# Performance work log

Measured on AMD Instinct MI355X. Metric: run time of the kernel, lower is better.

Reference implementation:

```python
import jax, jax.numpy as jnp
import numpy as np

H = 16  # hidden_size
I = 30  # GRU input_size (hard-coded in module)


def setup_inputs() -> dict:
    key = jax.random.key(0)
    ks = jax.random.split(key, 12)
    B, T = 4096, 512
    s = lambda k, sh: jax.random.normal(k, sh, jnp.float32) * 0.1
    return {
        "x": jax.random.normal(ks[0], (B, T, I), jnp.float32),
        "lengths": jax.random.randint(ks[1], (B,), 1, T + 1),  # valid lengths in [1, T]
        "w_ih": s(ks[2], (3 * H, I)),
        "w_hh": s(ks[3], (3 * H, H)),
        "b_ih": s(ks[4], (3 * H,)),
        "b_hh": s(ks[5], (3 * H,)),
        "fc1_w": s(ks[6], (H, H)), "fc1_b": s(ks[7], (H,)),
        "fc2_w": s(ks[8], (H, H)), "fc2_b": s(ks[9], (H,)),
        "fc3_w": s(ks[10], (H, H)), "fc3_b": s(ks[11], (H,)),
    }


def _gru_last_hidden(x, lengths, w_ih, w_hh, b_ih, b_hh):
    """Run GRU over padded [B,T,I] and return hidden at t = lengths-1 per row.
    Equivalent to pack_padded -> GRU -> pad_packed -> gather output[b, len-1],
    since h_t only depends on steps <= t."""
    B, T, _ = x.shape
    # Precompute input-side gate activations for all steps: [B,T,3H]
    xg = jnp.einsum('bti,gi->btg', x, w_ih) + b_ih
    xr, xz, xn = jnp.split(xg, 3, axis=-1)
    w_hr, w_hz, w_hn = jnp.split(w_hh, 3, axis=0)
    b_hr, b_hz, b_hn = jnp.split(b_hh, 3)
    tidx = lengths - 1  # [B]

    def step(carry, inp):
        h, last = carry
        t, xr_t, xz_t, xn_t = inp
        r = jax.nn.sigmoid(xr_t + h @ w_hr.T + b_hr)
        z = jax.nn.sigmoid(xz_t + h @ w_hz.T + b_hz)
        n = jnp.tanh(xn_t + r * (h @ w_hn.T + b_hn))
        h = (1.0 - z) * n + z * h
        last = jnp.where((tidx == t)[:, None], h, last)  # capture h at final valid step
        return (h, last), None

    h0 = jnp.zeros((B, H), x.dtype)
    (_, last), _ = jax.lax.scan(
        step, (h0, h0),
        (jnp.arange(T),
         xr.transpose(1, 0, 2), xz.transpose(1, 0, 2), xn.transpose(1, 0, 2)))
    return last  # [B,H]


def reference(x, lengths, w_ih, w_hh, b_ih, b_hh,
              fc1_w, fc1_b, fc2_w, fc2_b, fc3_w, fc3_b):
    h = _gru_last_hidden(x, lengths, w_ih, w_hh, b_ih, b_hh)
    e = h @ fc1_w.T + fc1_b
    e = jax.nn.relu(e) @ fc2_w.T + fc2_b   # dropout is identity in eval mode
    e = jax.nn.relu(e) @ fc3_w.T + fc3_b
    return e
```

## Files before the change

### kernel.cpp

```cpp
#include <hip/hip_runtime.h>
#include <cstdint>
#include <cstddef>

typedef float v2f __attribute__((ext_vector_type(2)));

#define HID 16
#define IN  30

#define FAST_RCP(x) __builtin_amdgcn_rcpf(x)

__device__ __forceinline__ float bperm(int baddr, float v) {
    return __int_as_float(__builtin_amdgcn_ds_bpermute(baddr, __float_as_int(v)));
}
__device__ __forceinline__ float dq1(float v) {
    return __int_as_float(__builtin_amdgcn_mov_dpp(__float_as_int(v), 0xB1, 0xF, 0xF, true));
}
__device__ __forceinline__ float dq2(float v) {
    return __int_as_float(__builtin_amdgcn_mov_dpp(__float_as_int(v), 0x4E, 0xF, 0xF, true));
}
#define PKFMA(acc, a, b) asm("v_pk_fma_f32 %0, %1, %2, %0" : "+v"(acc) : "v"(a), "v"(b))
#define PKMUL(d, a, b)   asm("v_pk_mul_f32 %0, %1, %2"     : "=v"(d)   : "v"(a), "v"(b))

typedef __attribute__((address_space(3))) unsigned int       lds_u32_t;
typedef const __attribute__((address_space(1))) unsigned int glb_u32_t;
#define GLOAD_LDS(gp, lp) \
    __builtin_amdgcn_global_load_lds((glb_u32_t*)(gp), (lds_u32_t*)(lp), 4, 0, 0)

__global__ void k_hist(const int* __restrict__ len, int* __restrict__ hist, int B, int T) {
    int i = blockIdx.x * 256 + threadIdx.x;
    if (i < B) atomicAdd(hist + (T - len[i]), 1);
}
__global__ __launch_bounds__(512) void k_scan(const int* __restrict__ hist, int* __restrict__ off) {
    __shared__ int s[512];
    int t = threadIdx.x;
    int v = hist[t];
    s[t] = v; __syncthreads();
    int acc = v;
    for (int o = 1; o < 512; o <<= 1) {
        int add = (t >= o) ? s[t - o] : 0;
        __syncthreads();
        acc += add; s[t] = acc;
        __syncthreads();
    }
    off[t] = acc - v;
}
__global__ void k_scatter(const int* __restrict__ len, int* __restrict__ off,
                          int* __restrict__ perm, int B, int T) {
    int i = blockIdx.x * 256 + threadIdx.x;
    if (i < B) {
        int b = T - len[i];
        int p = atomicAdd(off + b, 1);
        perm[p] = i;
    }
}

__global__ __launch_bounds__(256, 4) void gru_enc_kernel(
    const float* __restrict__ x, const int* __restrict__ lengths,
    const float* __restrict__ w_ih, const float* __restrict__ w_hh,
    const float* __restrict__ b_ih, const float* __restrict__ b_hh,
    const float* __restrict__ fc1w, const float* __restrict__ fc1b,
    const float* __restrict__ fc2w, const float* __restrict__ fc2b,
    const float* __restrict__ fc3w, const float* __restrict__ fc3b,
    float* __restrict__ out, const int* __restrict__ perm,
    int B, int T)
{
    __shared__ __align__(16) float lds[4][1024];

    const int lane = threadIdx.x & 63;
    const int wib  = threadIdx.x >> 6;
    const int q    = lane & 3;
    const int j    = lane >> 2;

    const int pos = blockIdx.x * 4 + wib;
    if (pos >= B) return;

    const int row = perm ? perm[pos] : pos;
    const int len = lengths[row];

    const float L2E = 1.4426950408889634f;
    const float gsc[3] = { -L2E, -L2E, 2.0f * L2E };

    v2f wih2[3][4];
#pragma unroll
    for (int g = 0; g < 3; ++g) {
        const float* wr = w_ih + (size_t)(g * HID + j) * IN;
#pragma unroll
        for (int m = 0; m < 4; ++m) {
            int p0 = q * 8 + 2 * m;
            v2f t;
            t.x = (p0     < IN) ? wr[p0]     * gsc[g] : 0.0f;
            t.y = (p0 + 1 < IN) ? wr[p0 + 1] * gsc[g] : 0.0f;
            wih2[g][m] = t;
        }
    }
    v2f whh2[3][2];
#pragma unroll
    for (int g = 0; g < 3; ++g)
#pragma unroll
        for (int m = 0; m < 2; ++m) {
            const float* wr = w_hh + (size_t)(g * HID + j) * HID + q * 4 + 2 * m;
            v2f t; t.x = wr[0] * gsc[g]; t.y = wr[1] * gsc[g];
            whh2[g][m] = t;
        }

    const float bR  = -L2E * (b_ih[j] + b_hh[j]);
    const float bZ  = -L2E * (b_ih[HID + j] + b_hh[HID + j]);
    const float biN = 2.0f * L2E * b_ih[2 * HID + j];
    const float bhN = 2.0f * L2E * b_hh[2 * HID + j];

    const int word  = min(lane & 31, 29);
    const int sstep = lane >> 5;
    const float* xrow = x + (size_t)row * T * IN;
    const int tcap = T - 1;

    float* ldsw = &lds[wib][0];
    const float* ldsr = ldsw + q * 8;

    int ba[4];
#pragma unroll
    for (int m = 0; m < 4; ++m) ba[m] = (16 * q + 4 * m) << 2;

#define STAGE(cc) do {                                                     \
        const int t0_ = (cc) << 3;                                         \
        float* lb_ = ldsw + (((cc) & 3) << 8);                             \
        _Pragma("unroll")                                                  \
        for (int i_ = 0; i_ < 4; ++i_) {                                   \
            int ts_ = min(t0_ + (i_ << 1) + sstep, tcap);                  \
            GLOAD_LDS(xrow + (size_t)ts_ * IN + word, lb_ + (i_ << 6));    \
        }                                                                  \
    } while (0)

#define STEP(cw, s) do {                                                    \
        v2f xv0 = *(const v2f*)((cw) + ((s) << 5));                         \
        v2f xv1 = *(const v2f*)((cw) + ((s) << 5) + 2);                     \
        v2f xv2 = *(const v2f*)((cw) + ((s) << 5) + 4);                     \
        v2f xv3 = *(const v2f*)((cw) + ((s) << 5) + 6);                     \
        v2f ar, az, an, hn;                                                 \
        PKMUL(ar, wih2[0][0], xv0);                                         \
        PKMUL(az, wih2[1][0], xv0);                                         \
        PKMUL(an, wih2[2][0], xv0);                                         \
        PKFMA(ar, wih2[0][1], xv1); PKFMA(az, wih2[1][1], xv1);             \
        PKFMA(an, wih2[2][1], xv1);                                         \
        PKFMA(ar, wih2[0][2], xv2); PKFMA(az, wih2[1][2], xv2);             \
        PKFMA(an, wih2[2][2], xv2);                                         \
        PKFMA(ar, wih2[0][3], xv3); PKFMA(az, wih2[1][3], xv3);             \
        PKFMA(an, wih2[2][3], xv3);                                         \
        PKMUL(hn, whh2[2][0], hb2[0]); PKFMA(hn, whh2[2][1], hb2[1]);       \
        PKFMA(ar, whh2[0][0], hb2[0]); PKFMA(ar, whh2[0][1], hb2[1]);       \
        PKFMA(az, whh2[1][0], hb2[0]); PKFMA(az, whh2[1][1], hb2[1]);       \
        float pr  = ar.x + ar.y;  pr  += dq1(pr);  pr  += dq2(pr);          \
        float pz  = az.x + az.y;  pz  += dq1(pz);  pz  += dq2(pz);          \
        float pxn = an.x + an.y;  pxn += dq1(pxn); pxn += dq2(pxn);         \
        float phn = hn.x + hn.y;  phn += dq1(phn); phn += dq2(phn);         \
        float rg = FAST_RCP(1.0f + __builtin_exp2f(pr + bR));               \
        float zg = FAST_RCP(1.0f + __builtin_exp2f(pz + bZ));               \
        float yy = fmaf(rg, phn + bhN, pxn + biN);                          \
        float ng = fmaf(-2.0f, FAST_RCP(1.0f + __builtin_exp2f(yy)), 1.0f); \
        h_own = fmaf(zg, h_own - ng, ng);                                   \
        hb2[0].x = bperm(ba[0], h_own); hb2[0].y = bperm(ba[1], h_own);     \
        hb2[1].x = bperm(ba[2], h_own); hb2[1].y = bperm(ba[3], h_own);     \
    } while (0)

    v2f hb2[2];
    hb2[0].x = 0.0f; hb2[0].y = 0.0f; hb2[1].x = 0.0f; hb2[1].y = 0.0f;
    float h_own = 0.0f;

    const int nfull = len >> 3;
    const int rem   = len & 7;

    STAGE(0); STAGE(1); STAGE(2);

    int c = 0;
    for (; c < nfull; ++c) {
        asm volatile("s_waitcnt vmcnt(8)" ::: "memory");
        STAGE(c + 3);
        const float* cw = ldsr + ((c & 3) << 8);
        STEP(cw, 0); STEP(cw, 1); STEP(cw, 2); STEP(cw, 3);
        STEP(cw, 4); STEP(cw, 5); STEP(cw, 6); STEP(cw, 7);
    }
    if (rem) {
        asm volatile("s_waitcnt vmcnt(8)" ::: "memory");
        const float* cw = ldsr + ((c & 3) << 8);
#pragma unroll
        for (int s = 0; s < 8; ++s) {
            if (s >= rem) break;
            STEP(cw, s);
        }
    }

    float hv[16];
#pragma unroll
    for (int k = 0; k < 16; ++k) hv[k] = __shfl(h_own, 4 * k, 64);

    float e1 = fc1b[j];
#pragma unroll
    for (int k = 0; k < 16; ++k) e1 = fmaf(fc1w[j * HID + k], hv[k], e1);

    float v1[16];
#pragma unroll
    for (int k = 0; k < 16; ++k) v1[k] = fmaxf(__shfl(e1, 4 * k, 64), 0.0f);

    float e2 = fc2b[j];
#pragma unroll
    for (int k = 0; k < 16; ++k) e2 = fmaf(fc2w[j * HID + k], v1[k], e2);

    float v2a[16];
#pragma unroll
    for (int k = 0; k < 16; ++k) v2a[k] = fmaxf(__shfl(e2, 4 * k, 64), 0.0f);

    float e3 = fc3b[j];
#pragma unroll
    for (int k = 0; k < 16; ++k) e3 = fmaf(fc3w[j * HID + k], v2a[k], e3);

    if (q == 0) out[(size_t)row * HID + j] = e3;
}

extern "C" void kernel_launch(void* const* d_in, const int* in_sizes, int n_in,
                              void* d_out, int out_size, void* d_ws, size_t ws_size,
                              hipStream_t stream) {
    const float* x    = (const float*)d_in[0];
    const int*   lens = (const int*)d_in[1];
    const float* w_ih = (const float*)d_in[2];
    const float* w_hh = (const float*)d_in[3];
    const float* b_ih = (const float*)d_in[4];
    const float* b_hh = (const float*)d_in[5];
    const float* fc1w = (const float*)d_in[6];
    const float* fc1b = (const float*)d_in[7];
    const float* fc2w = (const float*)d_in[8];
    const float* fc2b = (const float*)d_in[9];
    const float* fc3w = (const float*)d_in[10];
    const float* fc3b = (const float*)d_in[11];
    float* out = (float*)d_out;

    const int B = in_sizes[1];
    const int T = (int)(in_sizes[0] / ((size_t)B * IN));

    int* wsI = (int*)d_ws;
    const size_t need = ((size_t)B + 1024) * sizeof(int);
    const bool dosort = (ws_size >= need) && (T <= 512) && (T >= 8);
    int* perm = dosort ? wsI : nullptr;
    int* hist = wsI + B;
    int* off  = wsI + B + 512;

    if (dosort) {
        hipMemsetAsync(hist, 0, 512 * sizeof(int), stream);
        k_hist<<<(B + 255) / 256, 256, 0, stream>>>(lens, hist, B, T);
        k_scan<<<1, 512, 0, stream>>>(hist, off);
        k_scatter<<<(B + 255) / 256, 256, 0, stream>>>(lens, off, perm, B, T);
    }

    const int nblk = (B + 3) / 4;
    gru_enc_kernel<<<nblk, 256, 0, stream>>>(x, lens, w_ih, w_hh, b_ih, b_hh,
                                             fc1w, fc1b, fc2w, fc2b, fc3w, fc3b,
                                             out, perm, B, T);
}
```

Before: 173.1 us.

## Replace LDS-staged x pipeline with direct register prefetch, one wave per block

Drops the global_load_lds staging through shared memory and the vmcnt-gated 8-step chunk pipeline. Each lane now loads its own x slice straight into registers, prefetched four timesteps ahead in a rotating set of four buffers, and the q=3 lane's weights and offsets are remapped so no padding lanes are needed. Blocks shrink to a single 64-thread wave, one per batch row, removing the LDS footprint. The cost is more global load instructions per step issued from every lane, and latency hiding now rests on a four-step register prefetch depth.

After: 205.4 us. 1.19x slower.

```diff
diff --git a/kernel.cpp b/kernel.cpp
--- a/kernel.cpp
+++ b/kernel.cpp
@@ -20,11 +20,6 @@
 }
 #define PKFMA(acc, a, b) asm("v_pk_fma_f32 %0, %1, %2, %0" : "+v"(acc) : "v"(a), "v"(b))
 #define PKMUL(d, a, b)   asm("v_pk_mul_f32 %0, %1, %2"     : "=v"(d)   : "v"(a), "v"(b))
-
-typedef __attribute__((address_space(3))) unsigned int       lds_u32_t;
-typedef const __attribute__((address_space(1))) unsigned int glb_u32_t;
-#define GLOAD_LDS(gp, lp) \
-    __builtin_amdgcn_global_load_lds((glb_u32_t*)(gp), (lds_u32_t*)(lp), 4, 0, 0)
 
 __global__ void k_hist(const int* __restrict__ len, int* __restrict__ hist, int B, int T) {
     int i = blockIdx.x * 256 + threadIdx.x;
@@ -54,7 +49,7 @@
     }
 }
 
-__global__ __launch_bounds__(256, 4) void gru_enc_kernel(
+__global__ __launch_bounds__(64, 4) void gru_enc_kernel(
     const float* __restrict__ x, const int* __restrict__ lengths,
     const float* __restrict__ w_ih, const float* __restrict__ w_hh,
     const float* __restrict__ b_ih, const float* __restrict__ b_hh,
@@ -64,18 +59,16 @@
     float* __restrict__ out, const int* __restrict__ perm,
     int B, int T)
 {
-    __shared__ __align__(16) float lds[4][1024];
-
     const int lane = threadIdx.x & 63;
-    const int wib  = threadIdx.x >> 6;
     const int q    = lane & 3;
     const int j    = lane >> 2;
 
-    const int pos = blockIdx.x * 4 + wib;
+    const int pos = blockIdx.x;
     if (pos >= B) return;
 
     const int row = perm ? perm[pos] : pos;
     const int len = lengths[row];
+    const int lenm1 = len - 1;
 
     const float L2E = 1.4426950408889634f;
     const float gsc[3] = { -L2E, -L2E, 2.0f * L2E };
@@ -86,10 +79,15 @@
         const float* wr = w_ih + (size_t)(g * HID + j) * IN;
 #pragma unroll
         for (int m = 0; m < 4; ++m) {
-            int p0 = q * 8 + 2 * m;
+            int p0; bool zer = false;
+            if (q < 3) p0 = q * 8 + 2 * m;
+            else if (m == 0) p0 = 24;
+            else if (m == 1) p0 = 26;
+            else if (m == 2) { p0 = 0; zer = true; }
+            else p0 = 28;
             v2f t;
-            t.x = (p0     < IN) ? wr[p0]     * gsc[g] : 0.0f;
-            t.y = (p0 + 1 < IN) ? wr[p0 + 1] * gsc[g] : 0.0f;
+            t.x = zer ? 0.0f : wr[p0]     * gsc[g];
+            t.y = zer ? 0.0f : wr[p0 + 1] * gsc[g];
             wih2[g][m] = t;
         }
     }
@@ -108,43 +106,37 @@
     const float biN = 2.0f * L2E * b_ih[2 * HID + j];
     const float bhN = 2.0f * L2E * b_hh[2 * HID + j];
 
-    const int word  = min(lane & 31, 29);
-    const int sstep = lane >> 5;
-    const float* xrow = x + (size_t)row * T * IN;
-    const int tcap = T - 1;
-
-    float* ldsw = &lds[wib][0];
-    const float* ldsr = ldsw + q * 8;
-
-    int ba[4];
-#pragma unroll
-    for (int m = 0; m < 4; ++m) ba[m] = (16 * q + 4 * m) << 2;
-
-#define STAGE(cc) do {                                                     \
-        const int t0_ = (cc) << 3;                                         \
-        float* lb_ = ldsw + (((cc) & 3) << 8);                             \
-        _Pragma("unroll")                                                  \
-        for (int i_ = 0; i_ < 4; ++i_) {                                   \
-            int ts_ = min(t0_ + (i_ << 1) + sstep, tcap);                  \
-            GLOAD_LDS(xrow + (size_t)ts_ * IN + word, lb_ + (i_ << 6));    \
-        }                                                                  \
+    const int voff0 = (q < 3) ? q * 32      : 96;
+    const int voff1 = (q < 3) ? q * 32 + 8  : 104;
+    const int voff2 = (q < 3) ? q * 32 + 16 : 112;
+    const int voff3 = (q < 3) ? q * 32 + 24 : 112;
+
+    const char* xrow = (const char*)(x + (size_t)row * T * IN);
+
+    const int ba0 = (16 * q +  0) << 2;
+    const int ba1 = (16 * q +  4) << 2;
+    const int ba2 = (16 * q +  8) << 2;
+    const int ba3 = (16 * q + 12) << 2;
+
+#define LOADT(XB, tt) do {                                                  \
+        const char* p_ = xrow + (size_t)min((tt), lenm1) * (IN * 4);        \
+        XB[0] = *(const v2f*)(p_ + voff0);                                  \
+        XB[1] = *(const v2f*)(p_ + voff1);                                  \
+        XB[2] = *(const v2f*)(p_ + voff2);                                  \
+        XB[3] = *(const v2f*)(p_ + voff3);                                  \
     } while (0)
 
-#define STEP(cw, s) do {                                                    \
-        v2f xv0 = *(const v2f*)((cw) + ((s) << 5));                         \
-        v2f xv1 = *(const v2f*)((cw) + ((s) << 5) + 2);                     \
-        v2f xv2 = *(const v2f*)((cw) + ((s) << 5) + 4);                     \
-        v2f xv3 = *(const v2f*)((cw) + ((s) << 5) + 6);                     \
+#define STEP(XB) do {                                                       \
         v2f ar, az, an, hn;                                                 \
-        PKMUL(ar, wih2[0][0], xv0);                                         \
-        PKMUL(az, wih2[1][0], xv0);                                         \
-        PKMUL(an, wih2[2][0], xv0);                                         \
-        PKFMA(ar, wih2[0][1], xv1); PKFMA(az, wih2[1][1], xv1);             \
-        PKFMA(an, wih2[2][1], xv1);                                         \
-        PKFMA(ar, wih2[0][2], xv2); PKFMA(az, wih2[1][2], xv2);             \
-        PKFMA(an, wih2[2][2], xv2);                                         \
-        PKFMA(ar, wih2[0][3], xv3); PKFMA(az, wih2[1][3], xv3);             \
-        PKFMA(an, wih2[2][3], xv3);                                         \
+        PKMUL(ar, wih2[0][0], XB[0]);                                       \
+        PKMUL(az, wih2[1][0], XB[0]);                                       \
+        PKMUL(an, wih2[2][0], XB[0]);                                       \
+        PKFMA(ar, wih2[0][1], XB[1]); PKFMA(az, wih2[1][1], XB[1]);         \
+        PKFMA(an, wih2[2][1], XB[1]);                                       \
+        PKFMA(ar, wih2[0][2], XB[2]); PKFMA(az, wih2[1][2], XB[2]);         \
+        PKFMA(an, wih2[2][2], XB[2]);                                       \
+        PKFMA(ar, wih2[0][3], XB[3]); PKFMA(az, wih2[1][3], XB[3]);         \
+        PKFMA(an, wih2[2][3], XB[3]);                                       \
         PKMUL(hn, whh2[2][0], hb2[0]); PKFMA(hn, whh2[2][1], hb2[1]);       \
         PKFMA(ar, whh2[0][0], hb2[0]); PKFMA(ar, whh2[0][1], hb2[1]);       \
         PKFMA(az, whh2[1][0], hb2[0]); PKFMA(az, whh2[1][1], hb2[1]);       \
@@ -157,36 +149,27 @@
         float yy = fmaf(rg, phn + bhN, pxn + biN);                          \
         float ng = fmaf(-2.0f, FAST_RCP(1.0f + __builtin_exp2f(yy)), 1.0f); \
         h_own = fmaf(zg, h_own - ng, ng);                                   \
-        hb2[0].x = bperm(ba[0], h_own); hb2[0].y = bperm(ba[1], h_own);     \
-        hb2[1].x = bperm(ba[2], h_own); hb2[1].y = bperm(ba[3], h_own);     \
+        hb2[0].x = bperm(ba0, h_own); hb2[0].y = bperm(ba1, h_own);         \
+        hb2[1].x = bperm(ba2, h_own); hb2[1].y = bperm(ba3, h_own);         \
     } while (0)
 
     v2f hb2[2];
     hb2[0].x = 0.0f; hb2[0].y = 0.0f; hb2[1].x = 0.0f; hb2[1].y = 0.0f;
     float h_own = 0.0f;
 
-    const int nfull = len >> 3;
-    const int rem   = len & 7;
-
-    STAGE(0); STAGE(1); STAGE(2);
-
-    int c = 0;
-    for (; c < nfull; ++c) {
-        asm volatile("s_waitcnt vmcnt(8)" ::: "memory");
-        STAGE(c + 3);
-        const float* cw = ldsr + ((c & 3) << 8);
-        STEP(cw, 0); STEP(cw, 1); STEP(cw, 2); STEP(cw, 3);
-        STEP(cw, 4); STEP(cw, 5); STEP(cw, 6); STEP(cw, 7);
-    }
-    if (rem) {
-        asm volatile("s_waitcnt vmcnt(8)" ::: "memory");
-        const float* cw = ldsr + ((c & 3) << 8);
-#pragma unroll
-        for (int s = 0; s < 8; ++s) {
-            if (s >= rem) break;
-            STEP(cw, s);
-        }
-    }
+    v2f X0[4], X1[4], X2[4], X3[4];
+    LOADT(X0, 0); LOADT(X1, 1); LOADT(X2, 2); LOADT(X3, 3);
+
+    int t = 0;
+    for (; t + 4 <= len; t += 4) {
+        STEP(X0); LOADT(X0, t + 4);
+        STEP(X1); LOADT(X1, t + 5);
+        STEP(X2); LOADT(X2, t + 6);
+        STEP(X3); LOADT(X3, t + 7);
+    }
+    if (t     < len) STEP(X0);
+    if (t + 1 < len) STEP(X1);
+    if (t + 2 < len) STEP(X2);
 
     float hv[16];
 #pragma unroll
@@ -237,7 +220,7 @@
 
     int* wsI = (int*)d_ws;
     const size_t need = ((size_t)B + 1024) * sizeof(int);
-    const bool dosort = (ws_size >= need) && (T <= 512) && (T >= 8);
+    const bool dosort = (ws_size >= need) && (T <= 512) && (T >= 1);
     int* perm = dosort ? wsI : nullptr;
     int* hist = wsI + B;
     int* off  = wsI + B + 512;
@@ -249,8 +232,7 @@
         k_scatter<<<(B + 255) / 256, 256, 0, stream>>>(lens, off, perm, B, T);
     }
 
-    const int nblk = (B + 3) / 4;
-    gru_enc_kernel<<<nblk, 256, 0, stream>>>(x, lens, w_ih, w_hh, b_ih, b_hh,
-                                             fc1w, fc1b, fc2w, fc2b, fc3w, fc3b,
-                                             out, perm, B, T);
-}
+    gru_enc_kernel<<<B, 64, 0, stream>>>(x, lens, w_ih, w_hh, b_ih, b_hh,
+                                         fc1w, fc1b, fc2w, fc2b, fc3w, fc3b,
+                                         out, perm, B, T);
+}
```

## Broadcast hidden state via readlane and pair long/short rows per block

Applied to the files above, without the earlier changes.

Replaces the ds_bpermute exchange of the hidden state and the packed partial dot products with 16 v_readlane broadcasts into scalar registers. Each lane then computes a full 16-wide recurrent dot product per gate from weights held in registers, which removes the LDS-permute latency from the serial dependency chain. The trade-off is more VALU work and more registers per lane. Separately, each block now takes two rows from the front of the length-sorted order and two from the back, pairing long and short sequences so the work per block is more even. The duplicate guard on the back half looks questionable, and the sort is now also enabled for short T.

Result: slower. 298.3 us (+72.3%).

```diff
diff --git a/kernel.cpp b/kernel.cpp
--- a/kernel.cpp
+++ b/kernel.cpp
@@ -9,9 +9,6 @@
 
 #define FAST_RCP(x) __builtin_amdgcn_rcpf(x)
 
-__device__ __forceinline__ float bperm(int baddr, float v) {
-    return __int_as_float(__builtin_amdgcn_ds_bpermute(baddr, __float_as_int(v)));
-}
 __device__ __forceinline__ float dq1(float v) {
     return __int_as_float(__builtin_amdgcn_mov_dpp(__float_as_int(v), 0xB1, 0xF, 0xF, true));
 }
@@ -62,7 +59,7 @@
     const float* __restrict__ fc2w, const float* __restrict__ fc2b,
     const float* __restrict__ fc3w, const float* __restrict__ fc3b,
     float* __restrict__ out, const int* __restrict__ perm,
-    int B, int T)
+    int B, int T, int nblk)
 {
     __shared__ __align__(16) float lds[4][1024];
 
@@ -71,8 +68,11 @@
     const int q    = lane & 3;
     const int j    = lane >> 2;
 
-    const int pos = blockIdx.x * 4 + wib;
-    if (pos >= B) return;
+    int pos;
+    if (wib < 2) pos = 2 * blockIdx.x + wib;
+    else         pos = B - 2 - 2 * blockIdx.x + (wib - 2);
+    if (pos < 0 || pos >= B) return;
+    if (wib >= 2 && pos < 2 * nblk) return;
 
     const int row = perm ? perm[pos] : pos;
     const int len = lengths[row];
@@ -93,15 +93,12 @@
             wih2[g][m] = t;
         }
     }
-    v2f whh2[3][2];
+    float whh[3][16];
 #pragma unroll
     for (int g = 0; g < 3; ++g)
 #pragma unroll
-        for (int m = 0; m < 2; ++m) {
-            const float* wr = w_hh + (size_t)(g * HID + j) * HID + q * 4 + 2 * m;
-            v2f t; t.x = wr[0] * gsc[g]; t.y = wr[1] * gsc[g];
-            whh2[g][m] = t;
-        }
+        for (int k = 0; k < 16; ++k)
+            whh[g][k] = w_hh[(size_t)(g * HID + j) * HID + k] * gsc[g];
 
     const float bR  = -L2E * (b_ih[j] + b_hh[j]);
     const float bZ  = -L2E * (b_ih[HID + j] + b_hh[HID + j]);
@@ -115,10 +112,6 @@
 
     float* ldsw = &lds[wib][0];
     const float* ldsr = ldsw + q * 8;
-
-    int ba[4];
-#pragma unroll
-    for (int m = 0; m < 4; ++m) ba[m] = (16 * q + 4 * m) << 2;
 
 #define STAGE(cc) do {                                                     \
         const int t0_ = (cc) << 3;                                         \
@@ -130,12 +123,34 @@
         }                                                                  \
     } while (0)
 
+#define HDOT(res, g) do {                                                   \
+        float p0_ = whh[g][0] * hs0;                                        \
+        p0_ = fmaf(whh[g][1],  hs1,  p0_);                                  \
+        p0_ = fmaf(whh[g][2],  hs2,  p0_);                                  \
+        p0_ = fmaf(whh[g][3],  hs3,  p0_);                                  \
+        float p1_ = whh[g][4] * hs4;                                        \
+        p1_ = fmaf(whh[g][5],  hs5,  p1_);                                  \
+        p1_ = fmaf(whh[g][6],  hs6,  p1_);                                  \
+        p1_ = fmaf(whh[g][7],  hs7,  p1_);                                  \
+        float p2_ = whh[g][8] * hs8;                                        \
+        p2_ = fmaf(whh[g][9],  hs9,  p2_);                                  \
+        p2_ = fmaf(whh[g][10], hs10, p2_);                                  \
+        p2_ = fmaf(whh[g][11], hs11, p2_);                                  \
+        float p3_ = whh[g][12] * hs12;                                      \
+        p3_ = fmaf(whh[g][13], hs13, p3_);                                  \
+        p3_ = fmaf(whh[g][14], hs14, p3_);                                  \
+        p3_ = fmaf(whh[g][15], hs15, p3_);                                  \
+        res = (p0_ + p1_) + (p2_ + p3_);                                    \
+    } while (0)
+
+#define RDL(kk) __int_as_float(__builtin_amdgcn_readlane(__float_as_int(h_own), 4 * (kk)))
+
 #define STEP(cw, s) do {                                                    \
         v2f xv0 = *(const v2f*)((cw) + ((s) << 5));                         \
         v2f xv1 = *(const v2f*)((cw) + ((s) << 5) + 2);                     \
         v2f xv2 = *(const v2f*)((cw) + ((s) << 5) + 4);                     \
         v2f xv3 = *(const v2f*)((cw) + ((s) << 5) + 6);                     \
-        v2f ar, az, an, hn;                                                 \
+        v2f ar, az, an;                                                     \
         PKMUL(ar, wih2[0][0], xv0);                                         \
         PKMUL(az, wih2[1][0], xv0);                                         \
         PKMUL(an, wih2[2][0], xv0);                                         \
@@ -145,24 +160,26 @@
         PKFMA(an, wih2[2][2], xv2);                                         \
         PKFMA(ar, wih2[0][3], xv3); PKFMA(az, wih2[1][3], xv3);             \
         PKFMA(an, wih2[2][3], xv3);                                         \
-        PKMUL(hn, whh2[2][0], hb2[0]); PKFMA(hn, whh2[2][1], hb2[1]);       \
-        PKFMA(ar, whh2[0][0], hb2[0]); PKFMA(ar, whh2[0][1], hb2[1]);       \
-        PKFMA(az, whh2[1][0], hb2[0]); PKFMA(az, whh2[1][1], hb2[1]);       \
-        float pr  = ar.x + ar.y;  pr  += dq1(pr);  pr  += dq2(pr);          \
-        float pz  = az.x + az.y;  pz  += dq1(pz);  pz  += dq2(pz);          \
-        float pxn = an.x + an.y;  pxn += dq1(pxn); pxn += dq2(pxn);         \
-        float phn = hn.x + hn.y;  phn += dq1(phn); phn += dq2(phn);         \
-        float rg = FAST_RCP(1.0f + __builtin_exp2f(pr + bR));               \
-        float zg = FAST_RCP(1.0f + __builtin_exp2f(pz + bZ));               \
-        float yy = fmaf(rg, phn + bhN, pxn + biN);                          \
+        float xr = ar.x + ar.y;  xr += dq1(xr);  xr += dq2(xr);             \
+        float xz = az.x + az.y;  xz += dq1(xz);  xz += dq2(xz);             \
+        float xn = an.x + an.y;  xn += dq1(xn);  xn += dq2(xn);             \
+        float hr, hz, hn;                                                   \
+        HDOT(hr, 0); HDOT(hz, 1); HDOT(hn, 2);                              \
+        float rg = FAST_RCP(1.0f + __builtin_exp2f(xr + hr + bR));          \
+        float zg = FAST_RCP(1.0f + __builtin_exp2f(xz + hz + bZ));          \
+        float yy = fmaf(rg, hn + bhN, xn + biN);                            \
         float ng = fmaf(-2.0f, FAST_RCP(1.0f + __builtin_exp2f(yy)), 1.0f); \
         h_own = fmaf(zg, h_own - ng, ng);                                   \
-        hb2[0].x = bperm(ba[0], h_own); hb2[0].y = bperm(ba[1], h_own);     \
-        hb2[1].x = bperm(ba[2], h_own); hb2[1].y = bperm(ba[3], h_own);     \
+        hs0  = RDL(0);  hs1  = RDL(1);  hs2  = RDL(2);  hs3  = RDL(3);      \
+        hs4  = RDL(4);  hs5  = RDL(5);  hs6  = RDL(6);  hs7  = RDL(7);      \
+        hs8  = RDL(8);  hs9  = RDL(9);  hs10 = RDL(10); hs11 = RDL(11);     \
+        hs12 = RDL(12); hs13 = RDL(13); hs14 = RDL(14); hs15 = RDL(15);     \
     } while (0)
 
-    v2f hb2[2];
-    hb2[0].x = 0.0f; hb2[0].y = 0.0f; hb2[1].x = 0.0f; hb2[1].y = 0.0f;
+    float hs0 = 0.f, hs1 = 0.f, hs2 = 0.f, hs3 = 0.f;
+    float hs4 = 0.f, hs5 = 0.f, hs6 = 0.f, hs7 = 0.f;
+    float hs8 = 0.f, hs9 = 0.f, hs10 = 0.f, hs11 = 0.f;
+    float hs12 = 0.f, hs13 = 0.f, hs14 = 0.f, hs15 = 0.f;
     float h_own = 0.0f;
 
     const int nfull = len >> 3;
@@ -237,7 +254,7 @@
 
     int* wsI = (int*)d_ws;
     const size_t need = ((size_t)B + 1024) * sizeof(int);
-    const bool dosort = (ws_size >= need) && (T <= 512) && (T >= 8);
+    const bool dosort = (ws_size >= need) && (T <= 512) && (T >= 1);
     int* perm = dosort ? wsI : nullptr;
     int* hist = wsI + B;
     int* off  = wsI + B + 512;
@@ -252,5 +269,5 @@
     const int nblk = (B + 3) / 4;
     gru_enc_kernel<<<nblk, 256, 0, stream>>>(x, lens, w_ih, w_hh, b_ih, b_hh,
                                              fc1w, fc1b, fc2w, fc2b, fc3w, fc3b,
-                                             out, perm, B, T);
-}
+                                             out, perm, B, T, nblk);
+}
```
